# Optimization experiments

Measured on AMD Instinct MI355X. Metric: run time of the kernel, lower is better.

The kernel has to match this reference:

```python
import jax, jax.numpy as jnp
import numpy as np

HIDDEN = 1024
HEADS = 16
HEAD_DIM = 64
B, S = 2, 2048
SCALE = 1.0 / np.sqrt(HEAD_DIM)
NEG = -1e9


def setup_inputs() -> dict:
    key = jax.random.key(0)
    k1, k2, k3, k4, k5 = jax.random.split(key, 5)
    hidden_states = jax.random.normal(k1, (B, S, HIDDEN), dtype=jnp.float32)
    # causal additive mask, broadcast over heads: [B, 1, S, S]
    causal = jnp.where(jnp.tril(jnp.ones((S, S), dtype=bool)), 0.0, NEG).astype(jnp.float32)
    attention_mask = jnp.broadcast_to(causal[None, None], (B, 1, S, S))
    std = 1.0 / np.sqrt(HIDDEN)
    Wq = jax.random.normal(k2, (HIDDEN, HEADS * HEAD_DIM), dtype=jnp.float32) * std
    Wk = jax.random.normal(k3, (HIDDEN, HEADS * HEAD_DIM), dtype=jnp.float32) * std
    Wv = jax.random.normal(k4, (HIDDEN, HEADS * HEAD_DIM), dtype=jnp.float32) * std
    Wo = jax.random.normal(k5, (HEADS * HEAD_DIM, HIDDEN), dtype=jnp.float32) * std
    return {"hidden_states": hidden_states, "attention_mask": attention_mask,
            "Wq": Wq, "Wk": Wk, "Wv": Wv, "Wo": Wo}


def reference(hidden_states, attention_mask, Wq, Wk, Wv, Wo):
    b, s, _ = hidden_states.shape
    # projections (eval mode: dropouts are identity)
    q = (hidden_states @ Wq).reshape(b, s, HEADS, HEAD_DIM).transpose(0, 2, 1, 3)  # [B,H,S,D]
    k = (hidden_states @ Wk).reshape(b, s, HEADS, HEAD_DIM).transpose(0, 2, 1, 3)
    v = (hidden_states @ Wv).reshape(b, s, HEADS, HEAD_DIM).transpose(0, 2, 1, 3)
    scores = jnp.einsum('bhqd,bhkd->bhqk', q, k) * SCALE + attention_mask  # [B,H,S,S]
    probs = jax.nn.softmax(scores, axis=-1)
    out = jnp.einsum('bhqk,bhkd->bhqd', probs, v)  # [B,H,S,D]
    out = out.transpose(0, 2, 1, 3).reshape(b, s, HEADS * HEAD_DIM)
    return out @ Wo  # [B,S,HIDDEN]
```

## Files before the change

### kernel.cpp

```cpp
#include <hip/hip_runtime.h>

typedef unsigned short u16;
typedef unsigned int u32;
typedef __bf16 bf16x8 __attribute__((ext_vector_type(8)));
typedef float f32x4 __attribute__((ext_vector_type(4)));

#define MFMA(a, b, c) __builtin_amdgcn_mfma_f32_16x16x32_bf16(a, b, c, 0, 0, 0)

#define GLD16(gsrc, ldst)                                                          \
  __builtin_amdgcn_global_load_lds(                                                \
      (const __attribute__((address_space(1))) void*)(gsrc),                       \
      (__attribute__((address_space(3))) void*)(ldst), 16, 0, 0)

__device__ __forceinline__ u16 f2bf(float f) {
  u32 u = __builtin_bit_cast(u32, f);
  u32 r = (u + 0x7fffu + ((u >> 16) & 1u)) >> 16;
  return (u16)r;
}

__device__ __forceinline__ u32 pk2(float a, float b) {
  return (u32)f2bf(a) | ((u32)f2bf(b) << 16);
}

__device__ __forceinline__ float bf2f(u16 u) {
  return __builtin_bit_cast(float, ((u32)u) << 16);
}

__global__ __launch_bounds__(256) void k_cvt_x(const float* __restrict__ x,
                                               u16* __restrict__ xb) {
  int i = blockIdx.x * 256 + threadIdx.x;
  const float4* p = (const float4*)x + (size_t)i * 2;
  float4 a = p[0], b = p[1];
  uint4 o;
  o.x = pk2(a.x, a.y);
  o.y = pk2(a.z, a.w);
  o.z = pk2(b.x, b.y);
  o.w = pk2(b.z, b.w);
  *(uint4*)(xb + (size_t)i * 8) = o;
}

__global__ __launch_bounds__(256) void k_transpose_w(
    const float* __restrict__ Wq, const float* __restrict__ Wk,
    const float* __restrict__ Wv, const float* __restrict__ Wo,
    u16* __restrict__ Wt, u16* __restrict__ Wot) {
  __shared__ u16 t[32][33];
  const int k0 = blockIdx.x * 32, n0 = blockIdx.y * 32;
  const int x = threadIdx.x & 31, y = threadIdx.x >> 5;
  const float* src = (n0 < 1024) ? Wq : (n0 < 2048) ? Wk : (n0 < 3072) ? Wv : Wo;
  const int ncol = n0 & 1023;
#pragma unroll
  for (int rr = 0; rr < 4; ++rr) {
    int kl = y + rr * 8;
    t[x][kl] = f2bf(src[(size_t)(k0 + kl) * 1024 + ncol + x]);
  }
  __syncthreads();
  u16* dst = (n0 < 3072) ? (Wt + (size_t)n0 * 1024) : (Wot + (size_t)(n0 - 3072) * 1024);
#pragma unroll
  for (int rr = 0; rr < 4; ++rr) {
    int nl = y + rr * 8;
    dst[(size_t)nl * 1024 + k0 + x] = t[nl][x];
  }
}

__global__ __launch_bounds__(256) void k_gemm_qkv(const u16* __restrict__ A,
                                                  const u16* __restrict__ Bt,
                                                  u16* __restrict__ Q,
                                                  u16* __restrict__ K,
                                                  u16* __restrict__ Vt) {
  __shared__ u16 As[128 * 32];
  __shared__ u16 Bs[128 * 32];
  const int tid = threadIdx.x;
  const int w = tid >> 6, l = tid & 63;
  const int lr = l & 15, lg = l >> 4;
  const int lin = blockIdx.y * 24 + blockIdx.x;
  const int swz = (lin & 7) * 96 + (lin >> 3);
  const int tM = (swz / 24) * 128, tN = (swz % 24) * 128;
  const int wr = w >> 1, wc = w & 1;
  f32x4 acc[4][4] = {};

  for (int kk = 0; kk < 1024; kk += 32) {
#pragma unroll
    for (int j = 0; j < 2; ++j) {
      int rowA = tM + j * 64 + w * 16 + (l >> 2);
      GLD16(A + (size_t)rowA * 1024 + kk + (l & 3) * 8, As + (j * 64 + w * 16) * 32);
      int rowB = tN + j * 64 + w * 16 + (l >> 2);
      GLD16(Bt + (size_t)rowB * 1024 + kk + (l & 3) * 8, Bs + (j * 64 + w * 16) * 32);
    }
    __syncthreads();
    bf16x8 a[4], b[4];
#pragma unroll
    for (int m = 0; m < 4; ++m) a[m] = *(const bf16x8*)(As + (wr * 64 + m * 16 + lr) * 32 + lg * 8);
#pragma unroll
    for (int n = 0; n < 4; ++n) b[n] = *(const bf16x8*)(Bs + (wc * 64 + n * 16 + lr) * 32 + lg * 8);
#pragma unroll
    for (int m = 0; m < 4; ++m)
#pragma unroll
      for (int n = 0; n < 4; ++n) acc[m][n] = MFMA(a[m], b[n], acc[m][n]);
    __syncthreads();
  }

#pragma unroll
  for (int m = 0; m < 4; ++m) {
    int r0 = tM + wr * 64 + m * 16 + lg * 4;
    int b_ = r0 >> 11, s0 = r0 & 2047;
#pragma unroll
    for (int n = 0; n < 4; ++n) {
      int c = tN + wc * 64 + n * 16 + lr;
      int buf = c >> 10, c2 = c & 1023;
      int h = c2 >> 6, d = c2 & 63;
      if (buf == 2) {
        uint2 val;
        val.x = pk2(acc[m][n][0], acc[m][n][1]);
        val.y = pk2(acc[m][n][2], acc[m][n][3]);
        *(uint2*)(Vt + ((size_t)(b_ * 16 + h) * 64 + d) * 2048 + s0) = val;
      } else {
        u16* dst = (buf == 0) ? Q : K;
        float sc = (buf == 0) ? 0.125f : 1.0f;
#pragma unroll
        for (int j = 0; j < 4; ++j)
          dst[((size_t)(b_ * 16 + h) * 2048 + (s0 + j)) * 64 + d] = f2bf(acc[m][n][j] * sc);
      }
    }
  }
}

__global__ __launch_bounds__(256, 4) void k_attn(const u16* __restrict__ Q,
                                                 const u16* __restrict__ Kg,
                                                 const u16* __restrict__ Vtg,
                                                 u16* __restrict__ AO,
                                                 u16* __restrict__ PO,
                                                 float* __restrict__ ML) {
  __shared__ __align__(16) u16 Ks[2][64 * 64];
  __shared__ __align__(16) u16 Vs[2][64 * 64];
  __shared__ __align__(16) u16 Ps[4][16 * 64];
  const int tid = threadIdx.x;
  const int w = tid >> 6, l = tid & 63;
  const int lr = l & 15, lg = l >> 4;

  const int idx = blockIdx.x;
  const int bh = idx & 31;
  const int g = idx >> 5;
  int qt, c0;
  if (g < 16) { qt = 16 + g; c0 = 0; }
  else if (g < 32) { qt = 31 - (g - 16); c0 = 1; }
  else { qt = 15 - (g - 32); c0 = 0; }
  const int nkt = (qt < 16) ? (qt + 1) : (c0 == 0 ? 16 : qt - 15);
  const bool hasdiag = (qt < 16) || (c0 == 1);
  const int q0 = qt * 64;

  const u16* Qp = Q + (size_t)bh * 2048 * 64;
  const u16* Kp = Kg + (size_t)bh * 2048 * 64;
  const u16* Vp = Vtg + (size_t)bh * 64 * 2048;

  const int qrow = q0 + w * 16 + lr;
  bf16x8 qa0 = *(const bf16x8*)(Qp + (size_t)qrow * 64 + lg * 8);
  bf16x8 qa1 = *(const bf16x8*)(Qp + (size_t)qrow * 64 + 32 + lg * 8);

  f32x4 oacc[4] = {};
  float m_run = -1e30f, l_run = 0.f;

  const int srow = l >> 3;
  const int scol = ((l & 7) ^ srow) * 8;
  const int sw = (lr & 7) << 3;

  const u16* kptr = Kp + ((size_t)c0 * 1024 + srow) * 64 + scol;
  const u16* vptr = Vp + (size_t)srow * 2048 + c0 * 1024 + scol;

#pragma unroll
  for (int j = 0; j < 2; ++j) {
    int base = j * 32 + w * 8;
    GLD16(kptr + base * 64, &Ks[0][base * 64]);
    GLD16(vptr + (size_t)base * 2048, &Vs[0][base * 64]);
  }
  kptr += 4096;
  vptr += 64;
  __syncthreads();

  int cur = 0;

#define ATTN_TILE(DOPRE, DOMASK)                                                   \
  {                                                                                \
    if (DOPRE) {                                                                   \
      _Pragma("unroll") for (int j = 0; j < 2; ++j) {                              \
        int base = j * 32 + w * 8;                                                 \
        GLD16(kptr + base * 64, &Ks[cur ^ 1][base * 64]);                          \
        GLD16(vptr + (size_t)base * 2048, &Vs[cur ^ 1][base * 64]);                \
      }                                                                            \
      kptr += 4096;                                                                \
      vptr += 64;                                                                  \
    }                                                                              \
    f32x4 st[4];                                                                   \
    _Pragma("unroll") for (int n = 0; n < 4; ++n) {                                \
      const u16* kr = &Ks[cur][(n * 16 + lr) * 64];                                \
      bf16x8 kb0 = *(const bf16x8*)(kr + ((lg << 3) ^ sw));                        \
      bf16x8 kb1 = *(const bf16x8*)(kr + (((4 + lg) << 3) ^ sw));                  \
      f32x4 z = {0.f, 0.f, 0.f, 0.f};                                              \
      z = MFMA(kb0, qa0, z);                                                       \
      z = MFMA(kb1, qa1, z);                                                       \
      st[n] = z;                                                                   \
    }                                                                              \
    float mx = -1e30f;                                                             \
    _Pragma("unroll") for (int n = 0; n < 4; ++n)                                  \
        _Pragma("unroll") for (int j = 0; j < 4; ++j) {                            \
      float s = st[n][j];                                                          \
      if (DOMASK && (n * 16 + lg * 4 + j) > (w * 16 + lr)) s = -1e30f;             \
      st[n][j] = s;                                                                \
      mx = fmaxf(mx, s);                                                           \
    }                                                                              \
    mx = fmaxf(mx, __shfl_xor(mx, 16, 64));                                        \
    mx = fmaxf(mx, __shfl_xor(mx, 32, 64));                                        \
    const bool grow = __any(mx > m_run);                                           \
    float mnew = grow ? fmaxf(m_run, mx) : m_run;                                  \
    float rsum = 0.f;                                                              \
    _Pragma("unroll") for (int n = 0; n < 4; ++n)                                  \
        _Pragma("unroll") for (int j = 0; j < 4; ++j) {                            \
      float p = __expf(st[n][j] - mnew);                                           \
      st[n][j] = p;                                                                \
      rsum += p;                                                                   \
    }                                                                              \
    rsum += __shfl_xor(rsum, 16, 64);                                              \
    rsum += __shfl_xor(rsum, 32, 64);                                              \
    if (grow) {                                                                    \
      float fsc = __expf(m_run - mnew);                                            \
      l_run = l_run * fsc + rsum;                                                  \
      m_run = mnew;                                                                \
      float fscC[4];                                                               \
      _Pragma("unroll") for (int j = 0; j < 4; ++j) fscC[j] = __shfl(fsc, lg * 4 + j, 64); \
      _Pragma("unroll") for (int n = 0; n < 4; ++n)                                \
          _Pragma("unroll") for (int j = 0; j < 4; ++j) oacc[n][j] *= fscC[j];     \
    } else {                                                                       \
      l_run += rsum;                                                               \
    }                                                                              \
    u16* pb = &Ps[w][0];                                                           \
    _Pragma("unroll") for (int n = 0; n < 4; ++n) {                                \
      int slot = n * 2 + (lg >> 1);                                                \
      int off = lr * 64 + ((slot ^ (lr & 7)) << 3) + (lg & 1) * 4;                 \
      uint2 val;                                                                   \
      val.x = pk2(st[n][0], st[n][1]);                                             \
      val.y = pk2(st[n][2], st[n][3]);                                             \
      *(uint2*)(pb + off) = val;                                                   \
    }                                                                              \
    bf16x8 pa0 = *(const bf16x8*)(pb + lr * 64 + ((lg << 3) ^ sw));                \
    bf16x8 pa1 = *(const bf16x8*)(pb + lr * 64 + (((4 + lg) << 3) ^ sw));          \
    _Pragma("unroll") for (int n = 0; n < 4; ++n) {                                \
      const u16* vr = &Vs[cur][(n * 16 + lr) * 64];                                \
      bf16x8 vb0 = *(const bf16x8*)(vr + ((lg << 3) ^ sw));                        \
      bf16x8 vb1 = *(const bf16x8*)(vr + (((4 + lg) << 3) ^ sw));                  \
      oacc[n] = MFMA(pa0, vb0, oacc[n]);                                           \
      oacc[n] = MFMA(pa1, vb1, oacc[n]);                                           \
    }                                                                              \
  }

  for (int it = 0; it < nkt - 1; ++it) {
    ATTN_TILE(true, false);
    __syncthreads();
    cur ^= 1;
  }
  if (hasdiag) {
    ATTN_TILE(false, true);
  } else {
    ATTN_TILE(false, false);
  }
#undef ATTN_TILE

  if (qt < 16) {
    const int b_ = bh >> 4, h = bh & 15;
    float linv = 1.0f / l_run;
    float invC[4];
#pragma unroll
    for (int j = 0; j < 4; ++j) invC[j] = __shfl(linv, lg * 4 + j, 64);
#pragma unroll
    for (int j = 0; j < 4; ++j) {
      int s = q0 + w * 16 + lg * 4 + j;
#pragma unroll
      for (int n = 0; n < 4; ++n)
        AO[((size_t)(b_ * 2048 + s)) * 1024 + h * 64 + n * 16 + lr] = f2bf(oacc[n][j] * invC[j]);
    }
  } else {
    const int p = (bh * 16 + (qt - 16)) * 2 + c0;
    u16* po = PO + (size_t)p * 4096;
#pragma unroll
    for (int j = 0; j < 4; ++j) {
      int row = w * 16 + lg * 4 + j;
#pragma unroll
      for (int n = 0; n < 4; ++n) po[(size_t)row * 64 + n * 16 + lr] = f2bf(oacc[n][j]);
    }
    if (lg == 0) {
      ML[(size_t)p * 128 + (w * 16 + lr)] = m_run;
      ML[(size_t)p * 128 + 64 + (w * 16 + lr)] = l_run;
    }
  }
}

__global__ __launch_bounds__(256) void k_combine(const u16* __restrict__ PO,
                                                 const float* __restrict__ ML,
                                                 u16* __restrict__ AO) {
  const int blk = blockIdx.x;
  const int bh = blk >> 4, qt = 16 + (blk & 15);
  const int row = threadIdx.x >> 2;
  const int dseg = (threadIdx.x & 3) * 16;
  const size_t p0 = (size_t)blk * 2;
  const float m0 = ML[p0 * 128 + row], l0 = ML[p0 * 128 + 64 + row];
  const float m1 = ML[p0 * 128 + 128 + row], l1 = ML[p0 * 128 + 192 + row];
  const float M = fmaxf(m0, m1);
  float w0 = __expf(m0 - M), w1 = __expf(m1 - M);
  const float inv = 1.0f / (l0 * w0 + l1 * w1);
  w0 *= inv;
  w1 *= inv;
  const u16* o0 = PO + p0 * 4096 + (size_t)row * 64 + dseg;
  const u16* o1 = o0 + 4096;
  const int b_ = bh >> 4, h = bh & 15;
  u16* dst = AO + ((size_t)(b_ * 2048 + qt * 64 + row)) * 1024 + h * 64 + dseg;
#pragma unroll
  for (int half = 0; half < 2; ++half) {
    uint4 a = *(const uint4*)(o0 + half * 8);
    uint4 b = *(const uint4*)(o1 + half * 8);
    u32 aw[4] = {a.x, a.y, a.z, a.w};
    u32 bw[4] = {b.x, b.y, b.z, b.w};
    uint4 o;
    u32 ow[4];
#pragma unroll
    for (int i = 0; i < 4; ++i) {
      float r0 = bf2f((u16)(aw[i] & 0xffffu)) * w0 + bf2f((u16)(bw[i] & 0xffffu)) * w1;
      float r1 = bf2f((u16)(aw[i] >> 16)) * w0 + bf2f((u16)(bw[i] >> 16)) * w1;
      ow[i] = pk2(r0, r1);
    }
    o.x = ow[0]; o.y = ow[1]; o.z = ow[2]; o.w = ow[3];
    *(uint4*)(dst + half * 8) = o;
  }
}

__global__ __launch_bounds__(256) void k_gemm_out(const u16* __restrict__ A,
                                                  const u16* __restrict__ Bt,
                                                  float* __restrict__ out) {
  __shared__ u16 As[128 * 32];
  __shared__ u16 Bs[128 * 32];
  const int tid = threadIdx.x;
  const int w = tid >> 6, l = tid & 63;
  const int lr = l & 15, lg = l >> 4;
  const int lin = blockIdx.y * 8 + blockIdx.x;
  const int swz = (lin & 7) * 32 + (lin >> 3);
  const int tM = (swz / 8) * 128, tN = (swz % 8) * 128;
  const int wr = w >> 1, wc = w & 1;
  f32x4 acc[4][4] = {};

  for (int kk = 0; kk < 1024; kk += 32) {
#pragma unroll
    for (int j = 0; j < 2; ++j) {
      int rowA = tM + j * 64 + w * 16 + (l >> 2);
      GLD16(A + (size_t)rowA * 1024 + kk + (l & 3) * 8, As + (j * 64 + w * 16) * 32);
      int rowB = tN + j * 64 + w * 16 + (l >> 2);
      GLD16(Bt + (size_t)rowB * 1024 + kk + (l & 3) * 8, Bs + (j * 64 + w * 16) * 32);
    }
    __syncthreads();
    bf16x8 a[4], b[4];
#pragma unroll
    for (int m = 0; m < 4; ++m) a[m] = *(const bf16x8*)(As + (wr * 64 + m * 16 + lr) * 32 + lg * 8);
#pragma unroll
    for (int n = 0; n < 4; ++n) b[n] = *(const bf16x8*)(Bs + (wc * 64 + n * 16 + lr) * 32 + lg * 8);
#pragma unroll
    for (int m = 0; m < 4; ++m)
#pragma unroll
      for (int n = 0; n < 4; ++n) acc[m][n] = MFMA(a[m], b[n], acc[m][n]);
    __syncthreads();
  }

#pragma unroll
  for (int m = 0; m < 4; ++m) {
    int r0 = tM + wr * 64 + m * 16 + lg * 4;
#pragma unroll
    for (int n = 0; n < 4; ++n) {
      int c = tN + wc * 64 + n * 16 + lr;
#pragma unroll
      for (int j = 0; j < 4; ++j) out[(size_t)(r0 + j) * 1024 + c] = acc[m][n][j];
    }
  }
}

extern "C" void kernel_launch(void* const* d_in, const int* in_sizes, int n_in,
                              void* d_out, int out_size, void* d_ws, size_t ws_size,
                              hipStream_t stream) {
  const float* X = (const float*)d_in[0];
  const float* Wq = (const float*)d_in[2];
  const float* Wk = (const float*)d_in[3];
  const float* Wv = (const float*)d_in[4];
  const float* Wo = (const float*)d_in[5];
  float* out = (float*)d_out;

  char* ws = (char*)d_ws;
  if (ws_size < (size_t)48 * 1024 * 1024) return;
  u16* Xb  = (u16*)(ws);
  u16* Wt  = (u16*)(ws + 8388608);
  u16* Wot = (u16*)(ws + 14680064);
  u16* Q   = (u16*)(ws + 16777216);
  u16* K   = (u16*)(ws + 25165824);
  u16* Vt  = (u16*)(ws + 33554432);
  u16* AO  = (u16*)(ws + 41943040);
  u16*   PO = (u16*)(ws);
  float* ML = (float*)(ws + 8388608);

  k_cvt_x<<<2048, 256, 0, stream>>>(X, Xb);
  k_transpose_w<<<dim3(32, 128), 256, 0, stream>>>(Wq, Wk, Wv, Wo, Wt, Wot);
  k_gemm_qkv<<<dim3(24, 32), 256, 0, stream>>>(Xb, Wt, Q, K, Vt);
  k_attn<<<1536, 256, 0, stream>>>(Q, K, Vt, AO, PO, ML);
  k_combine<<<512, 256, 0, stream>>>(PO, ML, AO);
  k_gemm_out<<<dim3(8, 32), 256, 0, stream>>>(AO, Wot, out);
}
```

Baseline: 136.5 us.

## Double-buffer GEMM LDS tiles with XOR swizzle, vectorized stores, smaller out tiles

Both projection GEMMs now double-buffer their LDS tiles so the next k-slice is prefetched while the current one is computed. An XOR swizzle on the LDS column layout is meant to avoid bank conflicts. For Q/K and the output GEMM, the MFMA operands are swapped so each lane holds consecutive columns, which allows packed uint2/float4 stores instead of scalar scattered ones. The output GEMM moves to 128x64 tiles, doubling the block count for better occupancy, at the cost of more LDS use per block and more repeated A loads.

```diff
diff --git a/kernel.cpp b/kernel.cpp
--- a/kernel.cpp
+++ b/kernel.cpp
@@ -62,13 +62,14 @@
   }
 }
 
-__global__ __launch_bounds__(256) void k_gemm_qkv(const u16* __restrict__ A,
+
+__global__ __launch_bounds__(256) void k_gemm_qkv(const u16* __restrict__ A_,
                                                   const u16* __restrict__ Bt,
                                                   u16* __restrict__ Q,
                                                   u16* __restrict__ K,
                                                   u16* __restrict__ Vt) {
-  __shared__ u16 As[128 * 32];
-  __shared__ u16 Bs[128 * 32];
+  __shared__ __align__(16) u16 As[2][128 * 32];
+  __shared__ __align__(16) u16 Bs[2][128 * 32];
   const int tid = threadIdx.x;
   const int w = tid >> 6, l = tid & 63;
   const int lr = l & 15, lg = l >> 4;
@@ -76,52 +77,99 @@
   const int swz = (lin & 7) * 96 + (lin >> 3);
   const int tM = (swz / 24) * 128, tN = (swz % 24) * 128;
   const int wr = w >> 1, wc = w & 1;
+  const int bufsel = tN >> 10;
+
+  const int srow = l >> 2;
+  const int scol = (((l & 3) ^ ((l >> 3) & 3)) << 3);
+  const u16* Ag = A_ + (size_t)(tM + srow) * 1024 + scol;
+  const u16* Bg = Bt + (size_t)(tN + srow) * 1024 + scol;
+  const int rs = (lr >> 1) & 3;
+
+#define STAGE_QKV(buf, kk)                                                   \
+  {                                                                          \
+    GLD16(Ag + (size_t)(w * 16) * 1024 + (kk), &As[buf][(w * 16) * 32]);     \
+    GLD16(Ag + (size_t)(64 + w * 16) * 1024 + (kk), &As[buf][(64 + w * 16) * 32]); \
+    GLD16(Bg + (size_t)(w * 16) * 1024 + (kk), &Bs[buf][(w * 16) * 32]);     \
+    GLD16(Bg + (size_t)(64 + w * 16) * 1024 + (kk), &Bs[buf][(64 + w * 16) * 32]); \
+  }
+
   f32x4 acc[4][4] = {};
-
-  for (int kk = 0; kk < 1024; kk += 32) {
-#pragma unroll
-    for (int j = 0; j < 2; ++j) {
-      int rowA = tM + j * 64 + w * 16 + (l >> 2);
-      GLD16(A + (size_t)rowA * 1024 + kk + (l & 3) * 8, As + (j * 64 + w * 16) * 32);
-      int rowB = tN + j * 64 + w * 16 + (l >> 2);
-      GLD16(Bt + (size_t)rowB * 1024 + kk + (l & 3) * 8, Bs + (j * 64 + w * 16) * 32);
-    }
-    __syncthreads();
-    bf16x8 a[4], b[4];
-#pragma unroll
-    for (int m = 0; m < 4; ++m) a[m] = *(const bf16x8*)(As + (wr * 64 + m * 16 + lr) * 32 + lg * 8);
-#pragma unroll
-    for (int n = 0; n < 4; ++n) b[n] = *(const bf16x8*)(Bs + (wc * 64 + n * 16 + lr) * 32 + lg * 8);
-#pragma unroll
-    for (int m = 0; m < 4; ++m)
-#pragma unroll
-      for (int n = 0; n < 4; ++n) acc[m][n] = MFMA(a[m], b[n], acc[m][n]);
-    __syncthreads();
-  }
-
-#pragma unroll
-  for (int m = 0; m < 4; ++m) {
-    int r0 = tM + wr * 64 + m * 16 + lg * 4;
-    int b_ = r0 >> 11, s0 = r0 & 2047;
-#pragma unroll
-    for (int n = 0; n < 4; ++n) {
-      int c = tN + wc * 64 + n * 16 + lr;
-      int buf = c >> 10, c2 = c & 1023;
-      int h = c2 >> 6, d = c2 & 63;
-      if (buf == 2) {
+  STAGE_QKV(0, 0)
+  __syncthreads();
+  int cur = 0;
+
+  if (bufsel < 2) {
+    for (int t = 0; t < 32; ++t) {
+      if (t < 31) STAGE_QKV(cur ^ 1, (t + 1) * 32)
+      const u16* Ac = &As[cur][0];
+      const u16* Bc = &Bs[cur][0];
+      bf16x8 a[4], b[4];
+#pragma unroll
+      for (int m = 0; m < 4; ++m)
+        a[m] = *(const bf16x8*)(Ac + (wr * 64 + m * 16 + lr) * 32 + ((lg ^ rs) << 3));
+#pragma unroll
+      for (int n = 0; n < 4; ++n)
+        b[n] = *(const bf16x8*)(Bc + (wc * 64 + n * 16 + lr) * 32 + ((lg ^ rs) << 3));
+#pragma unroll
+      for (int m = 0; m < 4; ++m)
+#pragma unroll
+        for (int n = 0; n < 4; ++n) acc[m][n] = MFMA(b[n], a[m], acc[m][n]);
+      __syncthreads();
+      cur ^= 1;
+    }
+    u16* dst = bufsel ? K : Q;
+    const float sc = bufsel ? 1.0f : 0.125f;
+#pragma unroll
+    for (int m = 0; m < 4; ++m) {
+      int s = tM + wr * 64 + m * 16 + lr;
+      int b_ = s >> 11, sr2 = s & 2047;
+#pragma unroll
+      for (int n = 0; n < 4; ++n) {
+        int c = tN + wc * 64 + n * 16 + lg * 4;
+        int c2 = c & 1023;
+        int h = c2 >> 6, d = c2 & 63;
+        uint2 val;
+        val.x = pk2(acc[m][n][0] * sc, acc[m][n][1] * sc);
+        val.y = pk2(acc[m][n][2] * sc, acc[m][n][3] * sc);
+        *(uint2*)(dst + ((size_t)(b_ * 16 + h) * 2048 + sr2) * 64 + d) = val;
+      }
+    }
+  } else {
+    for (int t = 0; t < 32; ++t) {
+      if (t < 31) STAGE_QKV(cur ^ 1, (t + 1) * 32)
+      const u16* Ac = &As[cur][0];
+      const u16* Bc = &Bs[cur][0];
+      bf16x8 a[4], b[4];
+#pragma unroll
+      for (int m = 0; m < 4; ++m)
+        a[m] = *(const bf16x8*)(Ac + (wr * 64 + m * 16 + lr) * 32 + ((lg ^ rs) << 3));
+#pragma unroll
+      for (int n = 0; n < 4; ++n)
+        b[n] = *(const bf16x8*)(Bc + (wc * 64 + n * 16 + lr) * 32 + ((lg ^ rs) << 3));
+#pragma unroll
+      for (int m = 0; m < 4; ++m)
+#pragma unroll
+        for (int n = 0; n < 4; ++n) acc[m][n] = MFMA(a[m], b[n], acc[m][n]);
+      __syncthreads();
+      cur ^= 1;
+    }
+#pragma unroll
+    for (int m = 0; m < 4; ++m) {
+      int r0 = tM + wr * 64 + m * 16 + lg * 4;
+      int b_ = r0 >> 11, s0 = r0 & 2047;
+#pragma unroll
+      for (int n = 0; n < 4; ++n) {
+        int c = tN + wc * 64 + n * 16 + lr;
+        int c2 = c & 1023;
+        int h = c2 >> 6, d = c2 & 63;
         uint2 val;
         val.x = pk2(acc[m][n][0], acc[m][n][1]);
         val.y = pk2(acc[m][n][2], acc[m][n][3]);
         *(uint2*)(Vt + ((size_t)(b_ * 16 + h) * 64 + d) * 2048 + s0) = val;
-      } else {
-        u16* dst = (buf == 0) ? Q : K;
-        float sc = (buf == 0) ? 0.125f : 1.0f;
-#pragma unroll
-        for (int j = 0; j < 4; ++j)
-          dst[((size_t)(b_ * 16 + h) * 2048 + (s0 + j)) * 64 + d] = f2bf(acc[m][n][j] * sc);
       }
     }
   }
+#undef STAGE_QKV
 }
 
 __global__ __launch_bounds__(256, 4) void k_attn(const u16* __restrict__ Q,
@@ -330,49 +378,67 @@
   }
 }
 
-__global__ __launch_bounds__(256) void k_gemm_out(const u16* __restrict__ A,
+__global__ __launch_bounds__(256) void k_gemm_out(const u16* __restrict__ A_,
                                                   const u16* __restrict__ Bt,
                                                   float* __restrict__ out) {
-  __shared__ u16 As[128 * 32];
-  __shared__ u16 Bs[128 * 32];
+  __shared__ __align__(16) u16 As[2][128 * 32];
+  __shared__ __align__(16) u16 Bs[2][64 * 32];
   const int tid = threadIdx.x;
   const int w = tid >> 6, l = tid & 63;
   const int lr = l & 15, lg = l >> 4;
-  const int lin = blockIdx.y * 8 + blockIdx.x;
-  const int swz = (lin & 7) * 32 + (lin >> 3);
-  const int tM = (swz / 8) * 128, tN = (swz % 8) * 128;
-  const int wr = w >> 1, wc = w & 1;
-  f32x4 acc[4][4] = {};
-
-  for (int kk = 0; kk < 1024; kk += 32) {
-#pragma unroll
-    for (int j = 0; j < 2; ++j) {
-      int rowA = tM + j * 64 + w * 16 + (l >> 2);
-      GLD16(A + (size_t)rowA * 1024 + kk + (l & 3) * 8, As + (j * 64 + w * 16) * 32);
-      int rowB = tN + j * 64 + w * 16 + (l >> 2);
-      GLD16(Bt + (size_t)rowB * 1024 + kk + (l & 3) * 8, Bs + (j * 64 + w * 16) * 32);
-    }
+  const int lin = blockIdx.y * 16 + blockIdx.x;
+  const int swz = (lin & 7) * 64 + (lin >> 3);
+  const int tM = (swz / 16) * 128, tN = (swz % 16) * 64;
+
+  const int srow = l >> 2;
+  const int scol = (((l & 3) ^ ((l >> 3) & 3)) << 3);
+  const u16* Ag = A_ + (size_t)(tM + srow) * 1024 + scol;
+  const u16* Bg = Bt + (size_t)(tN + srow) * 1024 + scol;
+  const int rs = (lr >> 1) & 3;
+
+#define STAGE_OUT(buf, kk)                                                   \
+  {                                                                          \
+    GLD16(Ag + (size_t)(w * 16) * 1024 + (kk), &As[buf][(w * 16) * 32]);     \
+    GLD16(Ag + (size_t)(64 + w * 16) * 1024 + (kk), &As[buf][(64 + w * 16) * 32]); \
+    GLD16(Bg + (size_t)(w * 16) * 1024 + (kk), &Bs[buf][(w * 16) * 32]);     \
+  }
+
+  f32x4 acc[2][4] = {};
+  STAGE_OUT(0, 0)
+  __syncthreads();
+  int cur = 0;
+  for (int t = 0; t < 32; ++t) {
+    if (t < 31) STAGE_OUT(cur ^ 1, (t + 1) * 32)
+    const u16* Ac = &As[cur][0];
+    const u16* Bc = &Bs[cur][0];
+    bf16x8 a[2], b[4];
+#pragma unroll
+    for (int m = 0; m < 2; ++m)
+      a[m] = *(const bf16x8*)(Ac + (w * 32 + m * 16 + lr) * 32 + ((lg ^ rs) << 3));
+#pragma unroll
+    for (int n = 0; n < 4; ++n)
+      b[n] = *(const bf16x8*)(Bc + (n * 16 + lr) * 32 + ((lg ^ rs) << 3));
+#pragma unroll
+    for (int m = 0; m < 2; ++m)
+#pragma unroll
+      for (int n = 0; n < 4; ++n) acc[m][n] = MFMA(b[n], a[m], acc[m][n]);
     __syncthreads();
-    bf16x8 a[4], b[4];
-#pragma unroll
-    for (int m = 0; m < 4; ++m) a[m] = *(const bf16x8*)(As + (wr * 64 + m * 16 + lr) * 32 + lg * 8);
-#pragma unroll
-    for (int n = 0; n < 4; ++n) b[n] = *(const bf16x8*)(Bs + (wc * 64 + n * 16 + lr) * 32 + lg * 8);
-#pragma unroll
-    for (int m = 0; m < 4; ++m)
-#pragma unroll
-      for (int n = 0; n < 4; ++n) acc[m][n] = MFMA(a[m], b[n], acc[m][n]);
-    __syncthreads();
-  }
-
-#pragma unroll
-  for (int m = 0; m < 4; ++m) {
-    int r0 = tM + wr * 64 + m * 16 + lg * 4;
+    cur ^= 1;
+  }
+#undef STAGE_OUT
+
+#pragma unroll
+  for (int m = 0; m < 2; ++m) {
+    int s = tM + w * 32 + m * 16 + lr;
 #pragma unroll
     for (int n = 0; n < 4; ++n) {
-      int c = tN + wc * 64 + n * 16 + lr;
-#pragma unroll
-      for (int j = 0; j < 4; ++j) out[(size_t)(r0 + j) * 1024 + c] = acc[m][n][j];
+      int c = tN + n * 16 + lg * 4;
+      float4 v;
+      v.x = acc[m][n][0];
+      v.y = acc[m][n][1];
+      v.z = acc[m][n][2];
+      v.w = acc[m][n][3];
+      *(float4*)(out + (size_t)s * 1024 + c) = v;
     }
   }
 }
@@ -404,5 +470,5 @@
   k_gemm_qkv<<<dim3(24, 32), 256, 0, stream>>>(Xb, Wt, Q, K, Vt);
   k_attn<<<1536, 256, 0, stream>>>(Q, K, Vt, AO, PO, ML);
   k_combine<<<512, 256, 0, stream>>>(PO, ML, AO);
-  k_gemm_out<<<dim3(8, 32), 256, 0, stream>>>(AO, Wot, out);
-}
+  k_gemm_out<<<dim3(16, 32), 256, 0, stream>>>(AO, Wot, out);
+}
```

Measured after the change: 122.6 us. 1.11x faster.
